# Kernel optimization log

Measured on AMD Instinct MI355X. Metric: run time of the kernel, lower is better.

Reference implementation:

```python
import jax, jax.numpy as jnp
import numpy as np

E, H = 1024, 16
HD = E // H
QLEN, KLEN, BS = 1024, 2048, 4
PREV = KLEN - QLEN


def _rel_shift(x):
    # x: (q, k, b, h) -> Transformer-XL relative shift
    q, k, b, h = x.shape
    x = jnp.pad(x, ((0, 0), (1, 0), (0, 0), (0, 0)))  # (q, k+1, b, h)
    x = x.reshape(k + 1, q, b, h)[1:].reshape(q, k, b, h)
    return x


def setup_inputs() -> dict:
    key = jax.random.key(0)
    ks = jax.random.split(key, 16)
    s = 0.02  # weight init scale
    inp = {
        "query": jax.random.normal(ks[0], (QLEN, BS, E), jnp.float32),
        "key": jax.random.normal(ks[1], (KLEN, BS, E), jnp.float32),
        "value": jax.random.normal(ks[2], (KLEN, BS, E), jnp.float32),
        "pos_embedding": jax.random.normal(ks[3], (KLEN, 1, E), jnp.float32),
        "U": jax.random.normal(ks[4], (H, HD), jnp.float32) * s,
        "V": jax.random.normal(ks[5], (H, HD), jnp.float32) * s,
        "Wq": jax.random.normal(ks[6], (E, E), jnp.float32) * s,
        "bq": jnp.zeros((E,), jnp.float32),
        "Wk": jax.random.normal(ks[7], (E, E), jnp.float32) * s,
        "bk": jnp.zeros((E,), jnp.float32),
        "Wv": jax.random.normal(ks[8], (E, E), jnp.float32) * s,
        "bv": jnp.zeros((E,), jnp.float32),
        "Wp": jax.random.normal(ks[9], (E, E), jnp.float32) * s,
        "Wo": jax.random.normal(ks[10], (E, E), jnp.float32) * s,
        "bo": jnp.zeros((E,), jnp.float32),
    }
    # causal XL mask: query i attends to keys j <= i + PREV; True = masked
    qi = jnp.arange(QLEN)[:, None]
    kj = jnp.arange(KLEN)[None, :]
    inp["mask"] = (kj > qi + PREV)[:, :, None]  # (q, k, 1) bool
    return inp


def reference(query, key, value, pos_embedding, U, V, Wq, bq, Wk, bk, Wv, bv, Wp, Wo, bo, mask):
    q_len, b, e = query.shape
    k_len = key.shape[0]
    scale = float(np.sqrt(e))  # note: sqrt(embed_dim), as in the source

    queries = (query @ Wq + bq).reshape(q_len, b, H, HD)
    keys = (key @ Wk + bk).reshape(k_len, b, H, HD)
    values = (value @ Wv + bv).reshape(k_len, b, H, HD)
    R = (pos_embedding @ Wp).reshape(-1, H, HD)  # (k, H, HD)

    content_score = jnp.einsum('qbhd,kbhd->qkbh', queries + U, keys)
    position_score = jnp.einsum('qbhd,khd->qkbh', queries + V, R)
    position_score = _rel_shift(position_score)

    attention_score = (content_score + position_score) / scale
    attention_score = jnp.where(mask[..., None], jnp.float32(-1e20), attention_score)
    attention = jax.nn.softmax(attention_score, axis=1)

    alpha = jnp.einsum('qkbh,kbhd->qbhd', attention, values).reshape(q_len, b, e)
    return alpha @ Wo + bo
```

## Files before the change

kernel.cpp:

```cpp
#include <hip/hip_runtime.h>
#include <stdint.h>

#define QLEN 1024
#define KLEN 2048
#define BSZ  4
#define NH   16
#define HD   64
#define EMB  1024
#define PREVL 1024
#define SLOG2E 0.045084220027780106f

typedef __attribute__((ext_vector_type(4))) float f32x4;
typedef __attribute__((ext_vector_type(8))) short bf16x8;

__device__ __forceinline__ unsigned short f2bf(float f){
  unsigned u = __float_as_uint(f);
  u += 0x7fffu + ((u >> 16) & 1u);
  return (unsigned short)(u >> 16);
}

__device__ __forceinline__ void gload_lds16(const void* g, void* l){
  __builtin_amdgcn_global_load_lds((const __attribute__((address_space(1))) void*)g,
                                   (__attribute__((address_space(3))) void*)l, 16, 0, 0);
}

__global__ void txl_prep(const float* __restrict__ w0, const float* __restrict__ w1,
                         const float* __restrict__ w2, const float* __restrict__ w3,
                         const float* __restrict__ w4,
                         unsigned short* __restrict__ o0, unsigned short* __restrict__ o1,
                         unsigned short* __restrict__ o2, unsigned short* __restrict__ o3,
                         unsigned short* __restrict__ o4,
                         const float* __restrict__ q, const float* __restrict__ k,
                         const float* __restrict__ v, const float* __restrict__ p,
                         unsigned short* __restrict__ qo, unsigned short* __restrict__ ko,
                         unsigned short* __restrict__ vo, unsigned short* __restrict__ po){
  const int bid = blockIdx.x;
  if (bid < 5120){
    const int z = bid >> 10, rem = bid & 1023;
    const int by = rem >> 5, bx = rem & 31;
    const float* in; unsigned short* out;
    switch (z){
      case 0: in = w0; out = o0; break;
      case 1: in = w1; out = o1; break;
      case 2: in = w2; out = o2; break;
      case 3: in = w3; out = o3; break;
      default: in = w4; out = o4; break;
    }
    __shared__ float tile[32][33];
    int tx = threadIdx.x & 31, ty = threadIdx.x >> 5;
    int k0 = by * 32, n0 = bx * 32;
    #pragma unroll
    for (int j = 0; j < 32; j += 8)
      tile[ty + j][tx] = in[(size_t)(k0 + ty + j) * EMB + n0 + tx];
    __syncthreads();
    #pragma unroll
    for (int j = 0; j < 32; j += 8)
      out[(size_t)(n0 + ty + j) * EMB + k0 + tx] = f2bf(tile[tx][ty + j]);
  } else {
    for (size_t c = (size_t)(bid - 5120) * 256 + threadIdx.x; c < 2883584; c += (size_t)2048 * 256){
      const float* src; unsigned short* dst; size_t off;
      if (c < 524288)      { src = q; dst = qo; off = c; }
      else if (c < 1572864){ src = k; dst = ko; off = c - 524288; }
      else if (c < 2621440){ src = v; dst = vo; off = c - 1572864; }
      else                 { src = p; dst = po; off = c - 2621440; }
      f32x4 a = *(const f32x4*)(src + off * 8);
      f32x4 b = *(const f32x4*)(src + off * 8 + 4);
      bf16x8 r;
      #pragma unroll
      for (int u = 0; u < 4; ++u){ r[u] = (short)f2bf(a[u]); r[u + 4] = (short)f2bf(b[u]); }
      *(bf16x8*)(dst + off * 8) = r;
    }
  }
}

__global__ __launch_bounds__(256)
void txl_gemm_proj(const unsigned short* __restrict__ pbf, const unsigned short* __restrict__ qbf,
                   const unsigned short* __restrict__ kbf, const unsigned short* __restrict__ vbf,
                   const unsigned short* __restrict__ WpT, const unsigned short* __restrict__ WqT,
                   const unsigned short* __restrict__ WkT, const unsigned short* __restrict__ WvT,
                   const float* __restrict__ bq, const float* __restrict__ bk,
                   const float* __restrict__ bv, const float* __restrict__ U,
                   const float* __restrict__ V,
                   unsigned short* __restrict__ Rb, unsigned short* __restrict__ Qu,
                   unsigned short* __restrict__ Qv, unsigned short* __restrict__ Kb,
                   unsigned short* __restrict__ Vt){
  const int bid = blockIdx.x;
  int mode, local;
  const unsigned short *Ag, *Wt;
  if (bid < 128)      { mode = 3; local = bid;       Ag = pbf; Wt = WpT; }
  else if (bid < 384) { mode = 0; local = bid - 128; Ag = qbf; Wt = WqT; }
  else if (bid < 896) { mode = 1; local = bid - 384; Ag = kbf; Wt = WkT; }
  else                { mode = 2; local = bid - 896; Ag = vbf; Wt = WvT; }
  const int m0 = (local >> 3) * 128, n0 = (local & 7) * 128;

  const int tid = threadIdx.x;
  const int lane = tid & 63, wave = tid >> 6;
  const int lr = lane & 15, lg = lane >> 4;
  const int wm = wave >> 1, wn = wave & 1;
  __shared__ unsigned short At[128 * 64];
  __shared__ unsigned short Bt[128 * 64];
  f32x4 acc[4][4] = {};

  for (int kt = 0; kt < EMB / 64; ++kt){
    const int k0 = kt * 64;
    __syncthreads();
    #pragma unroll
    for (int j = 0; j < 4; ++j){
      int row = j * 32 + (tid >> 3);
      int g = (tid & 7) ^ (row & 7);
      gload_lds16(Ag + (size_t)(m0 + row) * EMB + k0 + g * 8, &At[j * 2048 + wave * 512]);
      gload_lds16(Wt + (size_t)(n0 + row) * EMB + k0 + g * 8, &Bt[j * 2048 + wave * 512]);
    }
    __syncthreads();
    #pragma unroll
    for (int ks = 0; ks < 2; ++ks){
      bf16x8 af[4], bfr[4];
      #pragma unroll
      for (int mb = 0; mb < 4; ++mb){
        int row = wm * 64 + mb * 16 + lr;
        af[mb] = *(const bf16x8*)&At[row * 64 + ((lg + 4 * ks) ^ (row & 7)) * 8];
      }
      #pragma unroll
      for (int nb = 0; nb < 4; ++nb){
        int row = wn * 64 + nb * 16 + lr;
        bfr[nb] = *(const bf16x8*)&Bt[row * 64 + ((lg + 4 * ks) ^ (row & 7)) * 8];
      }
      __builtin_amdgcn_s_setprio(1);
      #pragma unroll
      for (int mb = 0; mb < 4; ++mb)
        #pragma unroll
        for (int nb = 0; nb < 4; ++nb)
          acc[mb][nb] = __builtin_amdgcn_mfma_f32_16x16x32_bf16(af[mb], bfr[nb], acc[mb][nb], 0, 0, 0);
      __builtin_amdgcn_s_setprio(0);
    }
  }
  #pragma unroll
  for (int mb = 0; mb < 4; ++mb){
    #pragma unroll
    for (int nb = 0; nb < 4; ++nb){
      #pragma unroll
      for (int i = 0; i < 4; ++i){
        int m = m0 + wm * 64 + mb * 16 + 4 * lg + i;
        int n = n0 + wn * 64 + nb * 16 + lr;
        float v = acc[mb][nb][i];
        if (mode == 0){
          int qq = m >> 2, b = m & 3, h = n >> 6, d = n & 63;
          size_t idx = ((((size_t)b * NH + h) * QLEN) + qq) * HD + d;
          float base = v + bq[n];
          Qu[idx] = f2bf((base + U[n]) * SLOG2E);
          Qv[idx] = f2bf((base + V[n]) * SLOG2E);
        } else if (mode == 1){
          int kp = m >> 2, b = m & 3, h = n >> 6, d = n & 63;
          Kb[((((size_t)b * NH + h) * KLEN) + kp) * HD + d] = f2bf(v + bk[n]);
        } else if (mode == 2){
          int kp = m >> 2, b = m & 3, h = n >> 6, d = n & 63;
          Vt[((((size_t)b * NH + h) * HD) + d) * KLEN + kp] = f2bf(v + bv[n]);
        } else {
          int h = n >> 6, d = n & 63;
          Rb[((size_t)h * KLEN + m) * HD + d] = f2bf(v);
        }
      }
    }
  }
}

__global__ __launch_bounds__(256)
void txl_gemm_out(const unsigned short* __restrict__ Ag, const unsigned short* __restrict__ Wt,
                  const float* __restrict__ bias, float* __restrict__ out0){
  const int tid = threadIdx.x;
  const int lane = tid & 63, wave = tid >> 6;
  const int lr = lane & 15, lg = lane >> 4;
  const int wm = wave >> 1, wn = wave & 1;
  const int m0 = blockIdx.y * 128, n0 = blockIdx.x * 128;
  __shared__ unsigned short At[128 * 64];
  __shared__ unsigned short Bt[128 * 64];
  f32x4 acc[4][4] = {};

  for (int kt = 0; kt < EMB / 64; ++kt){
    const int k0 = kt * 64;
    __syncthreads();
    #pragma unroll
    for (int j = 0; j < 4; ++j){
      int row = j * 32 + (tid >> 3);
      int g = (tid & 7) ^ (row & 7);
      gload_lds16(Ag + (size_t)(m0 + row) * EMB + k0 + g * 8, &At[j * 2048 + wave * 512]);
      gload_lds16(Wt + (size_t)(n0 + row) * EMB + k0 + g * 8, &Bt[j * 2048 + wave * 512]);
    }
    __syncthreads();
    #pragma unroll
    for (int ks = 0; ks < 2; ++ks){
      bf16x8 af[4], bfr[4];
      #pragma unroll
      for (int mb = 0; mb < 4; ++mb){
        int row = wm * 64 + mb * 16 + lr;
        af[mb] = *(const bf16x8*)&At[row * 64 + ((lg + 4 * ks) ^ (row & 7)) * 8];
      }
      #pragma unroll
      for (int nb = 0; nb < 4; ++nb){
        int row = wn * 64 + nb * 16 + lr;
        bfr[nb] = *(const bf16x8*)&Bt[row * 64 + ((lg + 4 * ks) ^ (row & 7)) * 8];
      }
      __builtin_amdgcn_s_setprio(1);
      #pragma unroll
      for (int mb = 0; mb < 4; ++mb)
        #pragma unroll
        for (int nb = 0; nb < 4; ++nb)
          acc[mb][nb] = __builtin_amdgcn_mfma_f32_16x16x32_bf16(af[mb], bfr[nb], acc[mb][nb], 0, 0, 0);
      __builtin_amdgcn_s_setprio(0);
    }
  }
  #pragma unroll
  for (int mb = 0; mb < 4; ++mb)
    #pragma unroll
    for (int nb = 0; nb < 4; ++nb)
      #pragma unroll
      for (int i = 0; i < 4; ++i){
        int m = m0 + wm * 64 + mb * 16 + 4 * lg + i;
        int n = n0 + wn * 64 + nb * 16 + lr;
        out0[(size_t)m * EMB + n] = acc[mb][nb][i] + bias[n];
      }
}

__global__ __launch_bounds__(256)
void txl_attn(const unsigned short* __restrict__ Qu, const unsigned short* __restrict__ Qv,
              const unsigned short* __restrict__ Kb, const unsigned short* __restrict__ Vt,
              const unsigned short* __restrict__ Rb, unsigned short* __restrict__ alpha){
  const int tid = threadIdx.x, lane = tid & 63, wave = tid >> 6;
  const int lr = lane & 15, lg = lane >> 4;
  const int qt = 15 - blockIdx.x;
  const int h = blockIdx.y, b = blockIdx.z;
  const int q0 = qt * 64;
  const int myq0 = q0 + 16 * wave;

  __shared__ union { unsigned short q[2][64 * 64]; unsigned short p[4][16 * 64]; } smq;
  __shared__ unsigned short sm_k[64 * 64];
  __shared__ unsigned short sm_v[64 * 64];
  __shared__ unsigned short sm_r[128 * 64];
  __shared__ float sm_t[4][16 * 81];

  const unsigned short* quB = Qu + (((size_t)b * NH + h) * QLEN) * HD;
  const unsigned short* qvB = Qv + (((size_t)b * NH + h) * QLEN) * HD;
  const unsigned short* kB  = Kb + (((size_t)b * NH + h) * KLEN) * HD;
  const unsigned short* vB  = Vt + (((size_t)b * NH + h) * HD) * KLEN;
  const unsigned short* rB  = Rb + ((size_t)h * KLEN) * HD;

  #pragma unroll
  for (int j = 0; j < 2; ++j){
    int row = j * 32 + (tid >> 3);
    int g = (tid & 7) ^ (row & 7);
    gload_lds16(quB + (size_t)(q0 + row) * HD + g * 8, &smq.q[0][j * 2048 + wave * 512]);
    gload_lds16(qvB + (size_t)(q0 + row) * HD + g * 8, &smq.q[1][j * 2048 + wave * 512]);
  }
  __syncthreads();
  bf16x8 qfu[2], qfv[2];
  {
    int row = 16 * wave + lr;
    #pragma unroll
    for (int ks = 0; ks < 2; ++ks){
      qfu[ks] = *(const bf16x8*)&smq.q[0][row * 64 + ((lg + 4 * ks) ^ (row & 7)) * 8];
      qfv[ks] = *(const bf16x8*)&smq.q[1][row * 64 + ((lg + 4 * ks) ^ (row & 7)) * 8];
    }
  }

  f32x4 o[4] = {};
  float ls[4] = {0.f, 0.f, 0.f, 0.f};

  const int nk0 = qt + 17;
  const int nk = nk0 < 32 ? nk0 : 32;
  const int roff = 48 - 16 * wave;

  for (int kt = 0; kt < nk; ++kt){
    const int k0 = kt * 64;
    const int rbase = k0 + (QLEN - 64) - q0;
    __syncthreads();
    #pragma unroll
    for (int j = 0; j < 2; ++j){
      int row = j * 32 + (tid >> 3);
      int g = (tid & 7) ^ (row & 7);
      gload_lds16(kB + (size_t)(k0 + row) * HD + g * 8, &sm_k[j * 2048 + wave * 512]);
      gload_lds16(vB + (size_t)row * KLEN + k0 + g * 8, &sm_v[j * 2048 + wave * 512]);
    }
    #pragma unroll
    for (int j = 0; j < 4; ++j){
      int row = j * 32 + (tid >> 3);
      int g = (tid & 7) ^ (row & 7);
      int r = rbase + row; if (r > KLEN - 1) r = KLEN - 1;
      gload_lds16(rB + (size_t)r * HD + g * 8, &sm_r[j * 2048 + wave * 512]);
    }
    __syncthreads();

    f32x4 sc[4] = {};
    f32x4 tt[5] = {};
    __builtin_amdgcn_s_setprio(1);
    #pragma unroll
    for (int ks = 0; ks < 2; ++ks){
      #pragma unroll
      for (int nb = 0; nb < 4; ++nb){
        int row = nb * 16 + lr;
        bf16x8 kf = *(const bf16x8*)&sm_k[row * 64 + ((lg + 4 * ks) ^ (row & 7)) * 8];
        sc[nb] = __builtin_amdgcn_mfma_f32_16x16x32_bf16(qfu[ks], kf, sc[nb], 0, 0, 0);
      }
      #pragma unroll
      for (int rb = 0; rb < 5; ++rb){
        int row = roff + rb * 16 + lr;
        bf16x8 rf = *(const bf16x8*)&sm_r[row * 64 + ((lg + 4 * ks) ^ (row & 7)) * 8];
        tt[rb] = __builtin_amdgcn_mfma_f32_16x16x32_bf16(qfv[ks], rf, tt[rb], 0, 0, 0);
      }
    }
    __builtin_amdgcn_s_setprio(0);

    float* tw = sm_t[wave];
    #pragma unroll
    for (int rb = 0; rb < 5; ++rb)
      #pragma unroll
      for (int i = 0; i < 4; ++i)
        tw[(4 * lg + i) * 81 + rb * 16 + lr] = tt[rb][i];
    asm volatile("s_waitcnt lgkmcnt(0)" ::: "memory");

    #pragma unroll
    for (int i = 0; i < 4; ++i){
      int qq = 4 * lg + i;
      int qglob = myq0 + qq;
      float rs = 0.f;
      #pragma unroll
      for (int nb = 0; nb < 4; ++nb){
        int kk = nb * 16 + lr;
        float tv = tw[qq * 81 + kk + 15 - qq];
        float s = sc[nb][i] + tv;
        if (k0 + kk > qglob + PREVL) s = -1e30f;
        float p = exp2f(s);
        rs += p;
        smq.p[wave][qq * 64 + (((kk >> 3) ^ (qq & 7)) << 3) + (kk & 7)] = f2bf(p);
      }
      ls[i] += rs;
    }
    asm volatile("s_waitcnt lgkmcnt(0)" ::: "memory");

    __builtin_amdgcn_s_setprio(1);
    #pragma unroll
    for (int ks = 0; ks < 2; ++ks){
      bf16x8 pa = *(const bf16x8*)&smq.p[wave][lr * 64 + ((lg + 4 * ks) ^ (lr & 7)) * 8];
      #pragma unroll
      for (int db = 0; db < 4; ++db){
        int row = db * 16 + lr;
        bf16x8 vf = *(const bf16x8*)&sm_v[row * 64 + ((lg + 4 * ks) ^ (row & 7)) * 8];
        o[db] = __builtin_amdgcn_mfma_f32_16x16x32_bf16(pa, vf, o[db], 0, 0, 0);
      }
    }
    __builtin_amdgcn_s_setprio(0);
  }

  #pragma unroll
  for (int i = 0; i < 4; ++i){
    float s = ls[i];
    s += __shfl_xor(s, 1); s += __shfl_xor(s, 2);
    s += __shfl_xor(s, 4); s += __shfl_xor(s, 8);
    float inv = 1.0f / s;
    int q = myq0 + 4 * lg + i;
    #pragma unroll
    for (int db = 0; db < 4; ++db){
      int e = (h << 6) + db * 16 + lr;
      alpha[((size_t)q * BSZ + b) * EMB + e] = f2bf(o[db][i] * inv);
    }
  }
}

extern "C" void kernel_launch(void* const* d_in, const int* in_sizes, int n_in,
                              void* d_out, int out_size, void* d_ws, size_t ws_size,
                              hipStream_t stream) {
  const float* query = (const float*)d_in[0];
  const float* key   = (const float*)d_in[1];
  const float* value = (const float*)d_in[2];
  const float* pos   = (const float*)d_in[3];
  const float* U     = (const float*)d_in[4];
  const float* V     = (const float*)d_in[5];
  const float* Wq    = (const float*)d_in[6];
  const float* bq    = (const float*)d_in[7];
  const float* Wk    = (const float*)d_in[8];
  const float* bk    = (const float*)d_in[9];
  const float* Wv    = (const float*)d_in[10];
  const float* bv    = (const float*)d_in[11];
  const float* Wp    = (const float*)d_in[12];
  const float* Wo    = (const float*)d_in[13];
  const float* bo    = (const float*)d_in[14];

  char* w = (char*)d_ws;
  const size_t MB = 1u << 20;
  unsigned short* WqT = (unsigned short*)(w + 0 * MB);
  unsigned short* WkT = (unsigned short*)(w + 2 * MB);
  unsigned short* WvT = (unsigned short*)(w + 4 * MB);
  unsigned short* WpT = (unsigned short*)(w + 6 * MB);
  unsigned short* WoT = (unsigned short*)(w + 8 * MB);
  unsigned short* Qu  = (unsigned short*)(w + 10 * MB);
  unsigned short* Qv  = (unsigned short*)(w + 18 * MB);
  unsigned short* Kb  = (unsigned short*)(w + 26 * MB);
  unsigned short* Vt  = (unsigned short*)(w + 42 * MB);
  unsigned short* Rb  = (unsigned short*)(w + 58 * MB);
  unsigned short* qbf = (unsigned short*)(w + 62 * MB);
  unsigned short* kbf = (unsigned short*)(w + 70 * MB);
  unsigned short* vbf = (unsigned short*)(w + 86 * MB);
  unsigned short* pbf = (unsigned short*)(w + 102 * MB);
  unsigned short* alpha = qbf;

  txl_prep<<<dim3(7168), 256, 0, stream>>>(Wq, Wk, Wv, Wp, Wo, WqT, WkT, WvT, WpT, WoT,
                                           query, key, value, pos, qbf, kbf, vbf, pbf);

  txl_gemm_proj<<<dim3(1408), 256, 0, stream>>>(pbf, qbf, kbf, vbf, WpT, WqT, WkT, WvT,
                                                bq, bk, bv, U, V, Rb, Qu, Qv, Kb, Vt);

  txl_attn<<<dim3(16, 16, 4), 256, 0, stream>>>(Qu, Qv, Kb, Vt, Rb, alpha);

  txl_gemm_out<<<dim3(8, 32), 256, 0, stream>>>(alpha, WoT, bo, (float*)d_out);
}
```

Baseline: 284.7 us.

## Stage V-projection transpose through LDS and skip masking on interior tiles

The V-projection epilogue used to write each bf16 value to the transposed Vt layout with 2-byte stores strided by KLEN. It now stages the tile in shared memory, which is reused from the GEMM operand buffers through a union, and writes 16-byte rows that coalesce. The attention loop applies the causal mask only on the final key tile, since earlier tiles are fully visible, and drops a redundant clamp on the tile count. The cost is extra barriers and LDS traffic in the V epilogue.

```diff
diff --git a/kernel.cpp b/kernel.cpp
--- a/kernel.cpp
+++ b/kernel.cpp
@@ -97,8 +97,12 @@
   const int lane = tid & 63, wave = tid >> 6;
   const int lr = lane & 15, lg = lane >> 4;
   const int wm = wave >> 1, wn = wave & 1;
-  __shared__ unsigned short At[128 * 64];
-  __shared__ unsigned short Bt[128 * 64];
+  __shared__ union {
+    struct { unsigned short At[128 * 64]; unsigned short Bt[128 * 64]; } ab;
+    unsigned short tr[64 * 136];
+  } smem;
+  unsigned short* At = smem.ab.At;
+  unsigned short* Bt = smem.ab.Bt;
   f32x4 acc[4][4] = {};
 
   for (int kt = 0; kt < EMB / 64; ++kt){
@@ -134,30 +138,61 @@
       __builtin_amdgcn_s_setprio(0);
     }
   }
-  #pragma unroll
-  for (int mb = 0; mb < 4; ++mb){
-    #pragma unroll
-    for (int nb = 0; nb < 4; ++nb){
-      #pragma unroll
-      for (int i = 0; i < 4; ++i){
-        int m = m0 + wm * 64 + mb * 16 + 4 * lg + i;
-        int n = n0 + wn * 64 + nb * 16 + lr;
-        float v = acc[mb][nb][i];
-        if (mode == 0){
-          int qq = m >> 2, b = m & 3, h = n >> 6, d = n & 63;
-          size_t idx = ((((size_t)b * NH + h) * QLEN) + qq) * HD + d;
-          float base = v + bq[n];
-          Qu[idx] = f2bf((base + U[n]) * SLOG2E);
-          Qv[idx] = f2bf((base + V[n]) * SLOG2E);
-        } else if (mode == 1){
-          int kp = m >> 2, b = m & 3, h = n >> 6, d = n & 63;
-          Kb[((((size_t)b * NH + h) * KLEN) + kp) * HD + d] = f2bf(v + bk[n]);
-        } else if (mode == 2){
-          int kp = m >> 2, b = m & 3, h = n >> 6, d = n & 63;
-          Vt[((((size_t)b * NH + h) * HD) + d) * KLEN + kp] = f2bf(v + bv[n]);
-        } else {
-          int h = n >> 6, d = n & 63;
-          Rb[((size_t)h * KLEN + m) * HD + d] = f2bf(v);
+
+  if (mode == 2){
+    const int kp0 = m0 >> 2;
+    __syncthreads();
+    #pragma unroll
+    for (int pass = 0; pass < 2; ++pass){
+      if (wn == pass){
+        #pragma unroll
+        for (int mb = 0; mb < 4; ++mb){
+          int kp_l = wm * 16 + mb * 4 + lg;
+          #pragma unroll
+          for (int nb = 0; nb < 4; ++nb){
+            int nl = nb * 16 + lr;
+            float bvv = bv[n0 + pass * 64 + nl];
+            #pragma unroll
+            for (int i = 0; i < 4; ++i)
+              smem.tr[nl * 136 + i * 32 + kp_l] = f2bf(acc[mb][nb][i] + bvv);
+          }
+        }
+      }
+      __syncthreads();
+      #pragma unroll
+      for (int it = 0; it < 4; ++it){
+        int c = it * 256 + tid;
+        int nl = c >> 4, bb = (c >> 2) & 3, kpc = c & 3;
+        int n = n0 + pass * 64 + nl;
+        int hh = n >> 6, dd = n & 63;
+        bf16x8 vv = *(const bf16x8*)&smem.tr[nl * 136 + bb * 32 + kpc * 8];
+        *(bf16x8*)&Vt[((((size_t)bb * NH + hh) * HD) + dd) * KLEN + kp0 + kpc * 8] = vv;
+      }
+      __syncthreads();
+    }
+  } else {
+    #pragma unroll
+    for (int mb = 0; mb < 4; ++mb){
+      #pragma unroll
+      for (int nb = 0; nb < 4; ++nb){
+        #pragma unroll
+        for (int i = 0; i < 4; ++i){
+          int m = m0 + wm * 64 + mb * 16 + 4 * lg + i;
+          int n = n0 + wn * 64 + nb * 16 + lr;
+          float v = acc[mb][nb][i];
+          if (mode == 0){
+            int qq = m >> 2, b = m & 3, h = n >> 6, d = n & 63;
+            size_t idx = ((((size_t)b * NH + h) * QLEN) + qq) * HD + d;
+            float base = v + bq[n];
+            Qu[idx] = f2bf((base + U[n]) * SLOG2E);
+            Qv[idx] = f2bf((base + V[n]) * SLOG2E);
+          } else if (mode == 1){
+            int kp = m >> 2, b = m & 3, h = n >> 6, d = n & 63;
+            Kb[((((size_t)b * NH + h) * KLEN) + kp) * HD + d] = f2bf(v + bk[n]);
+          } else {
+            int h = n >> 6, d = n & 63;
+            Rb[((size_t)h * KLEN + m) * HD + d] = f2bf(v);
+          }
         }
       }
     }
@@ -265,8 +300,7 @@
   f32x4 o[4] = {};
   float ls[4] = {0.f, 0.f, 0.f, 0.f};
 
-  const int nk0 = qt + 17;
-  const int nk = nk0 < 32 ? nk0 : 32;
+  const int nk = qt + 17;
   const int roff = 48 - 16 * wave;
 
   for (int kt = 0; kt < nk; ++kt){
@@ -317,22 +351,37 @@
         tw[(4 * lg + i) * 81 + rb * 16 + lr] = tt[rb][i];
     asm volatile("s_waitcnt lgkmcnt(0)" ::: "memory");
 
-    #pragma unroll
-    for (int i = 0; i < 4; ++i){
-      int qq = 4 * lg + i;
-      int qglob = myq0 + qq;
-      float rs = 0.f;
-      #pragma unroll
-      for (int nb = 0; nb < 4; ++nb){
-        int kk = nb * 16 + lr;
-        float tv = tw[qq * 81 + kk + 15 - qq];
-        float s = sc[nb][i] + tv;
-        if (k0 + kk > qglob + PREVL) s = -1e30f;
-        float p = exp2f(s);
-        rs += p;
-        smq.p[wave][qq * 64 + (((kk >> 3) ^ (qq & 7)) << 3) + (kk & 7)] = f2bf(p);
-      }
-      ls[i] += rs;
+    if (kt + 1 < nk){
+      #pragma unroll
+      for (int i = 0; i < 4; ++i){
+        int qq = 4 * lg + i;
+        float rs = 0.f;
+        #pragma unroll
+        for (int nb = 0; nb < 4; ++nb){
+          int kk = nb * 16 + lr;
+          float p = exp2f(sc[nb][i] + tw[qq * 81 + kk + 15 - qq]);
+          rs += p;
+          smq.p[wave][qq * 64 + (((kk >> 3) ^ (qq & 7)) << 3) + (kk & 7)] = f2bf(p);
+        }
+        ls[i] += rs;
+      }
+    } else {
+      #pragma unroll
+      for (int i = 0; i < 4; ++i){
+        int qq = 4 * lg + i;
+        int qglob = myq0 + qq;
+        float rs = 0.f;
+        #pragma unroll
+        for (int nb = 0; nb < 4; ++nb){
+          int kk = nb * 16 + lr;
+          float s = sc[nb][i] + tw[qq * 81 + kk + 15 - qq];
+          if (k0 + kk > qglob + PREVL) s = -1e30f;
+          float p = exp2f(s);
+          rs += p;
+          smq.p[wave][qq * 64 + (((kk >> 3) ^ (qq & 7)) << 3) + (kk & 7)] = f2bf(p);
+        }
+        ls[i] += rs;
+      }
     }
     asm volatile("s_waitcnt lgkmcnt(0)" ::: "memory");
 
```

New measurement: 268.8 us. 1.06x faster.
